# Optimization experiments

Hardware: AMD Instinct MI355X
Metric: run time of the kernel (lower is better)

## Reference

```python
import jax, jax.numpy as jnp
import numpy as np

B, S, E, H = 4, 2048, 512, 8
D = E // H  # 64 per-head dim


def setup_inputs() -> dict:
    key = jax.random.key(0)
    kq, kk, kv, kwq, kwk, kwv, kwf, kbf = jax.random.split(key, 8)
    sc = 0.02
    return {
        "query": jax.random.normal(kq, (B, S, E), dtype=jnp.float32),
        "key": jax.random.normal(kk, (B, S, E), dtype=jnp.float32),
        "value": jax.random.normal(kv, (B, S, E), dtype=jnp.float32),
        "Wq": jax.random.normal(kwq, (D, D), dtype=jnp.float32) * sc,
        "Wk": jax.random.normal(kwk, (D, D), dtype=jnp.float32) * sc,
        "Wv": jax.random.normal(kwv, (D, D), dtype=jnp.float32) * sc,
        "Wfc": jax.random.normal(kwf, (E, E), dtype=jnp.float32) * sc,
        "bfc": jnp.zeros((E,), dtype=jnp.float32),
        "mask": jnp.tril(jnp.ones((1, 1, S, S), dtype=jnp.int32)),
    }


def reference(query, key, value, Wq, Wk, Wv, Wfc, bfc, mask):
    b, qlen, _ = query.shape
    klen = key.shape[1]
    # split heads: (B, L, H, D)
    q = query.reshape(b, qlen, H, D)
    k = key.reshape(b, klen, H, D)
    v = value.reshape(b, klen, H, D)
    # per-head linear projections (torch Linear: x @ W.T, no bias)
    q = jnp.einsum('bqhd,ed->bqhe', q, Wq)
    k = jnp.einsum('bkhd,ed->bkhe', k, Wk)
    v = jnp.einsum('bkhd,ed->bkhe', v, Wv)
    # full score matrix (B, H, Q, K)
    scores = jnp.einsum('bqhd,bkhd->bhqk', q, k)
    # faithful to source: mask-fill BEFORE dividing by sqrt(d)
    scores = jnp.where(mask == 0, jnp.float32(-1e20), scores)
    scores = scores / jnp.float32(np.sqrt(D))
    attn = jax.nn.softmax(scores, axis=-1)
    out = jnp.einsum('bhqk,bkhd->bqhd', attn, v).reshape(b, qlen, H * D)
    return out @ Wfc.T + bfc
```

## Files before the change

kernel.cpp:

```cpp
#include <hip/hip_runtime.h>
#include <hip/hip_bf16.h>

#define S_LEN 2048
#define EMB 512
#define NH 8
#define HD 64

#define AS1 __attribute__((address_space(1)))
#define AS3 __attribute__((address_space(3)))

typedef __bf16 bf16x8 __attribute__((ext_vector_type(8)));
typedef __bf16 bf16x4 __attribute__((ext_vector_type(4)));
typedef float f32x4 __attribute__((ext_vector_type(4)));
typedef float f32x16 __attribute__((ext_vector_type(16)));
typedef int i32x4 __attribute__((ext_vector_type(4)));

__device__ __forceinline__ unsigned swz(unsigned byteoff, unsigned row) {
    return byteoff ^ ((row & 7u) << 4);
}

__device__ __forceinline__ void plswap(int& a, int& b) {
#if __has_builtin(__builtin_amdgcn_permlane32_swap)
    auto r = __builtin_amdgcn_permlane32_swap(a, b, false, false);
    a = r[0];
    b = r[1];
#else
    asm("v_permlane32_swap_b32 %0, %1" : "+v"(a), "+v"(b));
#endif
}

__device__ __forceinline__ bf16x8 cvt8(const float* src) {
    float4 f0 = *reinterpret_cast<const float4*>(src);
    float4 f1 = *reinterpret_cast<const float4*>(src + 4);
    bf16x8 r;
    r[0] = (__bf16)f0.x; r[1] = (__bf16)f0.y; r[2] = (__bf16)f0.z; r[3] = (__bf16)f0.w;
    r[4] = (__bf16)f1.x; r[5] = (__bf16)f1.y; r[6] = (__bf16)f1.z; r[7] = (__bf16)f1.w;
    return r;
}

__global__ __launch_bounds__(256) void wcvt_kernel(
    const float* __restrict__ Wfc, const float* __restrict__ Wq,
    const float* __restrict__ Wk, const float* __restrict__ Wv,
    __bf16* __restrict__ Wb, __bf16* __restrict__ Wf)
{
    if (blockIdx.x < 128) {
        int i = (blockIdx.x * 256 + threadIdx.x) * 8;
        *reinterpret_cast<bf16x8*>(Wb + i) = cvt8(Wfc + i);
    } else {
        int s = (blockIdx.x - 128) * 256 + threadIdx.x;
        int p = s >> 9, rem = s & 511;
        int sub = rem >> 6, l = rem & 63;
        int nf = sub >> 1, ks = sub & 1;
        int col = l & 15, g = l >> 4;
        const float* Wsrc = (p == 0) ? Wq : (p == 1) ? Wk : Wv;
        *reinterpret_cast<bf16x8*>(Wf + (size_t)s * 8) =
            cvt8(Wsrc + (nf * 16 + col) * HD + ks * 32 + g * 8);
    }
}

__global__ __launch_bounds__(256) void proj_kernel(
    const float* __restrict__ qin, const float* __restrict__ kin, const float* __restrict__ vin,
    const __bf16* __restrict__ Wf,
    __bf16* __restrict__ Qp, __bf16* __restrict__ Kf, __bf16* __restrict__ Vf)
{
    __shared__ alignas(16) unsigned char xb[3][8192];
    __shared__ alignas(16) unsigned char tb[8192];
    const int bh = blockIdx.y;
    const int b = bh >> 3, h = bh & 7;
    const int sblk = blockIdx.x << 6;
    const int tid = threadIdx.x;
    const int w = tid >> 6, l = tid & 63;
    const int col = l & 15, g = l >> 4;
    const float K1 = 0.18033688011112042f;

    const float* srcs[3] = {qin, kin, vin};
    #pragma unroll
    for (int p = 0; p < 3; ++p) {
        const float* src = srcs[p] + ((size_t)b * S_LEN + sblk) * EMB + h * HD;
        #pragma unroll
        for (int it = 0; it < 4; ++it) {
            int c = tid + it * 256;
            int row = c >> 4, c4 = c & 15;
            float4 f = *reinterpret_cast<const float4*>(src + (size_t)row * EMB + c4 * 4);
            bf16x4 t;
            t[0] = (__bf16)f.x; t[1] = (__bf16)f.y; t[2] = (__bf16)f.z; t[3] = (__bf16)f.w;
            *reinterpret_cast<bf16x4*>(&xb[p][swz(row * 128 + c4 * 8, row)]) = t;
        }
    }
    __syncthreads();

    #pragma unroll
    for (int p = 0; p < 3; ++p) {
        bf16x8 wf[4][2];
        {
            const __bf16* wfb = Wf + p * 4096 + l * 8;
            #pragma unroll
            for (int nf = 0; nf < 4; ++nf)
                #pragma unroll
                for (int ks = 0; ks < 2; ++ks)
                    wf[nf][ks] = *reinterpret_cast<const bf16x8*>(wfb + (nf * 2 + ks) * 512);
        }
        int arow = w * 16 + col;
        bf16x8 a0 = *reinterpret_cast<const bf16x8*>(&xb[p][swz(arow * 128 + g * 16, arow)]);
        bf16x8 a1 = *reinterpret_cast<const bf16x8*>(&xb[p][swz(arow * 128 + 64 + g * 16, arow)]);
        f32x4 acc[4];
        #pragma unroll
        for (int nf = 0; nf < 4; ++nf) acc[nf] = (f32x4){0.f, 0.f, 0.f, 0.f};
        #pragma unroll
        for (int nf = 0; nf < 4; ++nf) {
            acc[nf] = __builtin_amdgcn_mfma_f32_16x16x32_bf16(a0, wf[nf][0], acc[nf], 0, 0, 0);
            acc[nf] = __builtin_amdgcn_mfma_f32_16x16x32_bf16(a1, wf[nf][1], acc[nf], 0, 0, 0);
        }
        const float s0 = (p == 0) ? K1 : 1.0f;
        #pragma unroll
        for (int nf = 0; nf < 4; ++nf)
            #pragma unroll
            for (int r = 0; r < 4; ++r) {
                int srow = w * 16 + g * 4 + r;
                unsigned tba = (unsigned)(srow * 128 + (nf * 16 + col) * 2) ^ ((srow & 7u) << 4);
                *reinterpret_cast<__bf16*>(&tb[tba]) = (__bf16)(acc[nf][r] * s0);
            }
        __syncthreads();
        if (p == 0) {
            int row = tid >> 2, eb = (tid & 3) * 32;
            bf16x8 v0 = *reinterpret_cast<const bf16x8*>(&tb[(unsigned)(row * 128 + eb) ^ ((row & 7u) << 4)]);
            bf16x8 v1 = *reinterpret_cast<const bf16x8*>(&tb[(unsigned)(row * 128 + eb + 16) ^ ((row & 7u) << 4)]);
            __bf16* dp = Qp + ((size_t)bh * S_LEN + sblk + row) * HD + eb / 2;
            *reinterpret_cast<bf16x8*>(dp) = v0;
            *reinterpret_cast<bf16x8*>(dp + 8) = v1;
        } else if (p == 1) {
            #pragma unroll
            for (int it = 0; it < 2; ++it) {
                int s = tid + it * 256;
                int Tloc = s >> 8, ks = (s >> 6) & 3, li = s & 63;
                int c32 = li & 31, h2 = li >> 5;
                int row = Tloc * 32 + c32;
                unsigned tba = (unsigned)(row * 128 + ks * 32 + h2 * 16) ^ ((row & 7u) << 4);
                bf16x8 v = *reinterpret_cast<const bf16x8*>(&tb[tba]);
                *reinterpret_cast<bf16x8*>(
                    Kf + (size_t)bh * 131072 +
                    ((size_t)(blockIdx.x * 2 + Tloc) * 4 + ks) * 512 + li * 8) = v;
            }
        } else {
            #pragma unroll
            for (int it = 0; it < 2; ++it) {
                int s = tid + it * 256;
                int Tloc = s >> 8, sub = (s >> 6) & 3, li = s & 63;
                int nf = sub >> 1, ks2 = sub & 1;
                int c32 = li & 31, h2 = li >> 5;
                int dcol = nf * 32 + c32;
                bf16x8 v;
                #pragma unroll
                for (int e = 0; e < 8; ++e) {
                    int row = Tloc * 32 + ks2 * 16 + h2 * 8 + e;
                    unsigned tba = (unsigned)(row * 128 + dcol * 2) ^ ((row & 7u) << 4);
                    v[e] = *reinterpret_cast<const __bf16*>(&tb[tba]);
                }
                *reinterpret_cast<bf16x8*>(
                    Vf + (size_t)bh * 131072 +
                    ((size_t)(blockIdx.x * 2 + Tloc) * 4 + sub) * 512 + li * 8) = v;
            }
        }
        __syncthreads();
    }
}

__global__ __launch_bounds__(256, 4) void attn_kernel(
    const __bf16* __restrict__ Qp, const __bf16* __restrict__ Kf,
    const __bf16* __restrict__ Vf, __bf16* __restrict__ Oa)
{
    __shared__ float mg[2][2112];
    const int l_id = blockIdx.x;
    const int bh = l_id & 31;
    const int pr = l_id >> 5;
    const int b = bh >> 3, h = bh & 7;
    const int tid = threadIdx.x;
    const int kh = tid >> 6;
    const int l = tid & 63;
    const int c32 = l & 31, hi = l >> 5;

    const __bf16* kbase = Kf + (size_t)bh * 131072;
    const __bf16* vbase = Vf + (size_t)bh * 131072;

    #pragma unroll 1
    for (int pass = 0; pass < 2; ++pass) {
        const int qt2 = pass ? 63 - pr : pr;

        bf16x8 qf[4];
        {
            const __bf16* qb = Qp + ((size_t)bh * S_LEN + qt2 * 32 + c32) * HD + hi * 8;
            #pragma unroll
            for (int ks = 0; ks < 4; ++ks)
                qf[ks] = *reinterpret_cast<const bf16x8*>(qb + ks * 16);
        }
        f32x16 oacc[2];
        #pragma unroll
        for (int nf = 0; nf < 2; ++nf)
            #pragma unroll
            for (int r = 0; r < 16; ++r) oacc[nf][r] = 0.f;
        float lsum = 0.f;

        const int cnt = (qt2 >= kh) ? ((qt2 - kh) >> 2) + 1 : 0;
        const bool has_mask = (kh == (qt2 & 3));
        const __bf16* kp = kbase + (size_t)kh * 2048 + l * 8;
        const __bf16* vp = vbase + (size_t)kh * 2048 + l * 8;

        #pragma unroll 1
        for (int i = 0; i < cnt; ++i) {
            f32x16 sfa;
            #pragma unroll
            for (int r = 0; r < 16; ++r) sfa[r] = -16.f;
            #pragma unroll
            for (int ks = 0; ks < 4; ++ks) {
                bf16x8 kf = *reinterpret_cast<const bf16x8*>(kp + ks * 512);
                sfa = __builtin_amdgcn_mfma_f32_32x32x16_bf16(kf, qf[ks], sfa, 0, 0, 0);
            }
            if (has_mask && i == cnt - 1) {
                #pragma unroll
                for (int r = 0; r < 16; ++r) {
                    int kvloc = (r & 3) + 8 * (r >> 2) + 4 * hi;
                    if (kvloc > c32) sfa[r] = -1e30f;
                }
            }
            float rsum = 0.f;
            int wds[8];
            #pragma unroll
            for (int i2 = 0; i2 < 8; ++i2) {
                float p0 = __builtin_exp2f(sfa[2 * i2]);
                float p1 = __builtin_exp2f(sfa[2 * i2 + 1]);
                rsum += p0 + p1;
                asm("v_cvt_pk_bf16_f32 %0, %1, %2" : "=v"(wds[i2]) : "v"(p0), "v"(p1));
            }
            lsum += rsum;
            plswap(wds[0], wds[2]);
            plswap(wds[1], wds[3]);
            plswap(wds[4], wds[6]);
            plswap(wds[5], wds[7]);
            #pragma unroll
            for (int nf = 0; nf < 2; ++nf) {
                #pragma unroll
                for (int ks2 = 0; ks2 < 2; ++ks2) {
                    i32x4 pw;
                    pw[0] = wds[ks2 * 4 + 0];
                    pw[1] = wds[ks2 * 4 + 1];
                    pw[2] = wds[ks2 * 4 + 2];
                    pw[3] = wds[ks2 * 4 + 3];
                    bf16x8 pfk = *reinterpret_cast<bf16x8*>(&pw);
                    bf16x8 vf = *reinterpret_cast<const bf16x8*>(vp + (nf * 2 + ks2) * 512);
                    oacc[nf] = __builtin_amdgcn_mfma_f32_32x32x16_bf16(vf, pfk, oacc[nf], 0, 0, 0);
                }
            }
            kp += 8192;
            vp += 8192;
        }

        __syncthreads();
        if (kh & 1) {
            float* bp = mg[kh >> 1];
            #pragma unroll
            for (int nf = 0; nf < 2; ++nf)
                #pragma unroll
                for (int r = 0; r < 16; ++r)
                    bp[(nf * 16 + r) * 64 + l] = oacc[nf][r];
            bp[2048 + l] = lsum;
        }
        __syncthreads();
        if (!(kh & 1)) {
            const float* bp = mg[kh >> 1];
            lsum += bp[2048 + l];
            #pragma unroll
            for (int nf = 0; nf < 2; ++nf)
                #pragma unroll
                for (int r = 0; r < 16; ++r)
                    oacc[nf][r] += bp[(nf * 16 + r) * 64 + l];
        }
        __syncthreads();
        if (kh == 2) {
            float* bp = mg[0];
            #pragma unroll
            for (int nf = 0; nf < 2; ++nf)
                #pragma unroll
                for (int r = 0; r < 16; ++r)
                    bp[(nf * 16 + r) * 64 + l] = oacc[nf][r];
            bp[2048 + l] = lsum;
        }
        __syncthreads();
        if (kh == 0) {
            const float* bp = mg[0];
            lsum += bp[2048 + l];
            #pragma unroll
            for (int nf = 0; nf < 2; ++nf)
                #pragma unroll
                for (int r = 0; r < 16; ++r)
                    oacc[nf][r] += bp[(nf * 16 + r) * 64 + l];
            lsum += __shfl_xor(lsum, 32);
            float inv = 1.0f / lsum;
            const int q = qt2 * 32 + c32;
            __bf16* op = Oa + ((size_t)b * S_LEN + q) * EMB + h * HD;
            #pragma unroll
            for (int nf = 0; nf < 2; ++nf)
                #pragma unroll
                for (int rq = 0; rq < 4; ++rq) {
                    bf16x4 o4;
                    #pragma unroll
                    for (int e = 0; e < 4; ++e)
                        o4[e] = (__bf16)(oacc[nf][rq * 4 + e] * inv);
                    *reinterpret_cast<bf16x4*>(op + nf * 32 + rq * 8 + hi * 4) = o4;
                }
        }
    }
}

__global__ __launch_bounds__(512) void fc_kernel(
    const __bf16* __restrict__ A,
    const __bf16* __restrict__ Wb,
    const float* __restrict__ bfc,
    float* __restrict__ out)
{
    __shared__ alignas(16) unsigned char smem[65536];
    const int tid = threadIdx.x;
    const int w = tid >> 6, l = tid & 63;
    const int c32 = l & 31, hi = l >> 5;
    const int mw = w >> 2, nw = w & 3;
    const int r0 = blockIdx.x * 128, n0 = blockIdx.y * 128;

    int sro[2], sof[2];
    #pragma unroll
    for (int j = 0; j < 2; ++j) {
        int s = w * 128 + j * 64 + l;
        int row = s >> 3, off = (s & 7) * 16;
        sro[j] = row;
        sof[j] = off ^ ((row & 7) << 4);
    }
    const unsigned char* Ag = reinterpret_cast<const unsigned char*>(A) + (size_t)r0 * 1024;
    const unsigned char* Wg = reinterpret_cast<const unsigned char*>(Wb) + (size_t)n0 * 1024;

    f32x16 oacc[2];
    #pragma unroll
    for (int nf = 0; nf < 2; ++nf)
        #pragma unroll
        for (int r = 0; r < 16; ++r) oacc[nf][r] = 0.f;

    #pragma unroll
    for (int j = 0; j < 2; ++j) {
        __builtin_amdgcn_global_load_lds(
            (const AS1 unsigned int*)(Ag + (size_t)sro[j] * 1024 + sof[j]),
            (AS3 unsigned int*)(smem + w * 2048 + j * 1024), 16, 0, 0);
        __builtin_amdgcn_global_load_lds(
            (const AS1 unsigned int*)(Wg + (size_t)sro[j] * 1024 + sof[j]),
            (AS3 unsigned int*)(smem + 16384 + w * 2048 + j * 1024), 16, 0, 0);
    }
    __syncthreads();

    int cur = 0;
    #pragma unroll 1
    for (int kc = 0; kc < 8; ++kc) {
        if (kc + 1 < 8) {
            unsigned char* Abn = smem + (cur ^ 1) * 32768;
            #pragma unroll
            for (int j = 0; j < 2; ++j) {
                __builtin_amdgcn_global_load_lds(
                    (const AS1 unsigned int*)(Ag + (size_t)sro[j] * 1024 + (kc + 1) * 128 + sof[j]),
                    (AS3 unsigned int*)(Abn + w * 2048 + j * 1024), 16, 0, 0);
                __builtin_amdgcn_global_load_lds(
                    (const AS1 unsigned int*)(Wg + (size_t)sro[j] * 1024 + (kc + 1) * 128 + sof[j]),
                    (AS3 unsigned int*)(Abn + 16384 + w * 2048 + j * 1024), 16, 0, 0);
            }
        }
        unsigned char* Ab = smem + cur * 32768;
        unsigned char* Wbuf = Ab + 16384;
        const int brow = nw * 32 + c32;
        #pragma unroll
        for (int ks = 0; ks < 4; ++ks) {
            bf16x8 bfg = *reinterpret_cast<const bf16x8*>(
                Wbuf + swz(brow * 128 + ks * 32 + hi * 16, brow));
            #pragma unroll
            for (int nf = 0; nf < 2; ++nf) {
                int arow = mw * 64 + nf * 32 + c32;
                bf16x8 afg = *reinterpret_cast<const bf16x8*>(
                    Ab + swz(arow * 128 + ks * 32 + hi * 16, arow));
                oacc[nf] = __builtin_amdgcn_mfma_f32_32x32x16_bf16(afg, bfg, oacc[nf], 0, 0, 0);
            }
        }
        __syncthreads();
        cur ^= 1;
    }

    const float bias = bfc[n0 + nw * 32 + c32];
    const int ncol = n0 + nw * 32 + c32;
    #pragma unroll
    for (int nf = 0; nf < 2; ++nf)
        #pragma unroll
        for (int r = 0; r < 16; ++r) {
            int mrow = r0 + mw * 64 + nf * 32 + (r & 3) + 8 * (r >> 2) + 4 * hi;
            out[(size_t)mrow * EMB + ncol] = oacc[nf][r] + bias;
        }
}

extern "C" void kernel_launch(void* const* d_in, const int* in_sizes, int n_in,
                              void* d_out, int out_size, void* d_ws, size_t ws_size,
                              hipStream_t stream) {
    const float* q   = (const float*)d_in[0];
    const float* k   = (const float*)d_in[1];
    const float* v   = (const float*)d_in[2];
    const float* Wq  = (const float*)d_in[3];
    const float* Wk  = (const float*)d_in[4];
    const float* Wv  = (const float*)d_in[5];
    const float* Wfc = (const float*)d_in[6];
    const float* bfc = (const float*)d_in[7];
    float* out = (float*)d_out;

    char* ws = (char*)d_ws;
    const size_t SZ = (size_t)4 * NH * S_LEN * HD * sizeof(__bf16);
    __bf16* Qp = (__bf16*)(ws);
    __bf16* Kf = (__bf16*)(ws + SZ);
    __bf16* Vf = (__bf16*)(ws + 2 * SZ);
    __bf16* Oa = (__bf16*)(ws + 3 * SZ);
    __bf16* Wb = (__bf16*)(ws + 4 * SZ);
    __bf16* Wf = (__bf16*)(ws + 4 * SZ + 524288);

    wcvt_kernel<<<dim3(134), 256, 0, stream>>>(Wfc, Wq, Wk, Wv, Wb, Wf);
    proj_kernel<<<dim3(S_LEN / 64, 4 * NH), 256, 0, stream>>>(q, k, v, Wf, Qp, Kf, Vf);
    attn_kernel<<<dim3(32 * 32), 256, 0, stream>>>(Qp, Kf, Vf, Oa);
    fc_kernel<<<dim3((4 * S_LEN) / 128, EMB / 128), 512, 0, stream>>>(Oa, Wb, bfc, out);
}
```

Before: 69.81 us.

## Store Q in fragment layout and software-prefetch K/V tiles in attention loop

Q is now written by the projection kernel in the same MFMA fragment layout as K, so the attention kernel loads Q fragments with contiguous 16-byte per-lane reads. The attention inner loop issues V loads at the start of each iteration and prefetches the next K tile right after the QK MFMAs, so global-load latency overlaps with the softmax and PV work. This raises register pressure from the extra in-flight K and V fragments, which could affect occupancy under the 4-blocks launch bound.

```diff
diff --git a/kernel.cpp b/kernel.cpp
--- a/kernel.cpp
+++ b/kernel.cpp
@@ -61,7 +61,7 @@
 __global__ __launch_bounds__(256) void proj_kernel(
     const float* __restrict__ qin, const float* __restrict__ kin, const float* __restrict__ vin,
     const __bf16* __restrict__ Wf,
-    __bf16* __restrict__ Qp, __bf16* __restrict__ Kf, __bf16* __restrict__ Vf)
+    __bf16* __restrict__ Qf, __bf16* __restrict__ Kf, __bf16* __restrict__ Vf)
 {
     __shared__ alignas(16) unsigned char xb[3][8192];
     __shared__ alignas(16) unsigned char tb[8192];
@@ -121,14 +121,8 @@
                 *reinterpret_cast<__bf16*>(&tb[tba]) = (__bf16)(acc[nf][r] * s0);
             }
         __syncthreads();
-        if (p == 0) {
-            int row = tid >> 2, eb = (tid & 3) * 32;
-            bf16x8 v0 = *reinterpret_cast<const bf16x8*>(&tb[(unsigned)(row * 128 + eb) ^ ((row & 7u) << 4)]);
-            bf16x8 v1 = *reinterpret_cast<const bf16x8*>(&tb[(unsigned)(row * 128 + eb + 16) ^ ((row & 7u) << 4)]);
-            __bf16* dp = Qp + ((size_t)bh * S_LEN + sblk + row) * HD + eb / 2;
-            *reinterpret_cast<bf16x8*>(dp) = v0;
-            *reinterpret_cast<bf16x8*>(dp + 8) = v1;
-        } else if (p == 1) {
+        if (p < 2) {
+            __bf16* dst = (p == 0) ? Qf : Kf;
             #pragma unroll
             for (int it = 0; it < 2; ++it) {
                 int s = tid + it * 256;
@@ -138,7 +132,7 @@
                 unsigned tba = (unsigned)(row * 128 + ks * 32 + h2 * 16) ^ ((row & 7u) << 4);
                 bf16x8 v = *reinterpret_cast<const bf16x8*>(&tb[tba]);
                 *reinterpret_cast<bf16x8*>(
-                    Kf + (size_t)bh * 131072 +
+                    dst + (size_t)bh * 131072 +
                     ((size_t)(blockIdx.x * 2 + Tloc) * 4 + ks) * 512 + li * 8) = v;
             }
         } else {
@@ -166,7 +160,7 @@
 }
 
 __global__ __launch_bounds__(256, 4) void attn_kernel(
-    const __bf16* __restrict__ Qp, const __bf16* __restrict__ Kf,
+    const __bf16* __restrict__ Qf, const __bf16* __restrict__ Kf,
     const __bf16* __restrict__ Vf, __bf16* __restrict__ Oa)
 {
     __shared__ float mg[2][2112];
@@ -188,10 +182,10 @@
 
         bf16x8 qf[4];
         {
-            const __bf16* qb = Qp + ((size_t)bh * S_LEN + qt2 * 32 + c32) * HD + hi * 8;
+            const __bf16* qb = Qf + (size_t)bh * 131072 + (size_t)qt2 * 2048 + l * 8;
             #pragma unroll
             for (int ks = 0; ks < 4; ++ks)
-                qf[ks] = *reinterpret_cast<const bf16x8*>(qb + ks * 16);
+                qf[ks] = *reinterpret_cast<const bf16x8*>(qb + ks * 512);
         }
         f32x16 oacc[2];
         #pragma unroll
@@ -205,15 +199,29 @@
         const __bf16* kp = kbase + (size_t)kh * 2048 + l * 8;
         const __bf16* vp = vbase + (size_t)kh * 2048 + l * 8;
 
+        bf16x8 kcur[4];
+        if (cnt > 0) {
+            #pragma unroll
+            for (int ks = 0; ks < 4; ++ks)
+                kcur[ks] = *reinterpret_cast<const bf16x8*>(kp + ks * 512);
+        }
+
         #pragma unroll 1
         for (int i = 0; i < cnt; ++i) {
+            bf16x8 vcur[4];
+            #pragma unroll
+            for (int j = 0; j < 4; ++j)
+                vcur[j] = *reinterpret_cast<const bf16x8*>(vp + j * 512);
             f32x16 sfa;
             #pragma unroll
             for (int r = 0; r < 16; ++r) sfa[r] = -16.f;
             #pragma unroll
-            for (int ks = 0; ks < 4; ++ks) {
-                bf16x8 kf = *reinterpret_cast<const bf16x8*>(kp + ks * 512);
-                sfa = __builtin_amdgcn_mfma_f32_32x32x16_bf16(kf, qf[ks], sfa, 0, 0, 0);
+            for (int ks = 0; ks < 4; ++ks)
+                sfa = __builtin_amdgcn_mfma_f32_32x32x16_bf16(kcur[ks], qf[ks], sfa, 0, 0, 0);
+            if (i + 1 < cnt) {
+                #pragma unroll
+                for (int ks = 0; ks < 4; ++ks)
+                    kcur[ks] = *reinterpret_cast<const bf16x8*>(kp + 8192 + ks * 512);
             }
             if (has_mask && i == cnt - 1) {
                 #pragma unroll
@@ -246,8 +254,8 @@
                     pw[2] = wds[ks2 * 4 + 2];
                     pw[3] = wds[ks2 * 4 + 3];
                     bf16x8 pfk = *reinterpret_cast<bf16x8*>(&pw);
-                    bf16x8 vf = *reinterpret_cast<const bf16x8*>(vp + (nf * 2 + ks2) * 512);
-                    oacc[nf] = __builtin_amdgcn_mfma_f32_32x32x16_bf16(vf, pfk, oacc[nf], 0, 0, 0);
+                    oacc[nf] = __builtin_amdgcn_mfma_f32_32x32x16_bf16(
+                        vcur[nf * 2 + ks2], pfk, oacc[nf], 0, 0, 0);
                 }
             }
             kp += 8192;
@@ -412,7 +420,7 @@
 
     char* ws = (char*)d_ws;
     const size_t SZ = (size_t)4 * NH * S_LEN * HD * sizeof(__bf16);
-    __bf16* Qp = (__bf16*)(ws);
+    __bf16* Qf = (__bf16*)(ws);
     __bf16* Kf = (__bf16*)(ws + SZ);
     __bf16* Vf = (__bf16*)(ws + 2 * SZ);
     __bf16* Oa = (__bf16*)(ws + 3 * SZ);
@@ -420,7 +428,7 @@
     __bf16* Wf = (__bf16*)(ws + 4 * SZ + 524288);
 
     wcvt_kernel<<<dim3(134), 256, 0, stream>>>(Wfc, Wq, Wk, Wv, Wb, Wf);
-    proj_kernel<<<dim3(S_LEN / 64, 4 * NH), 256, 0, stream>>>(q, k, v, Wf, Qp, Kf, Vf);
-    attn_kernel<<<dim3(32 * 32), 256, 0, stream>>>(Qp, Kf, Vf, Oa);
+    proj_kernel<<<dim3(S_LEN / 64, 4 * NH), 256, 0, stream>>>(q, k, v, Wf, Qf, Kf, Vf);
+    attn_kernel<<<dim3(32 * 32), 256, 0, stream>>>(Qf, Kf, Vf, Oa);
     fc_kernel<<<dim3((4 * S_LEN) / 128, EMB / 128), 512, 0, stream>>>(Oa, Wb, bfc, out);
 }
```

New measurement: 67.95 us. 2.7% less time.
